# Kernel tuning notes

Measured on AMD Instinct MI355X. Metric: run time of the kernel, lower is better.

## Reference

```python
import jax, jax.numpy as jnp
import numpy as np

DIM = 1024
HEADS = 16
DIM_HEAD = 64
INNER = HEADS * DIM_HEAD
SCALE = 8.0  # default scale in plain_cosine_sim_attention
EPS = 1e-5


def setup_inputs() -> dict:
    key = jax.random.key(0)
    ks = jax.random.split(key, 5)
    b, n = 2, 2048
    x = jax.random.normal(ks[0], (b, n, DIM), dtype=jnp.float32)
    ln_w = jnp.ones((DIM,), dtype=jnp.float32)
    ln_b = jnp.zeros((DIM,), dtype=jnp.float32)
    W_qkv = jax.random.normal(ks[1], (DIM, 3 * INNER), dtype=jnp.float32) * (DIM ** -0.5)
    W_out = jax.random.normal(ks[2], (INNER, DIM), dtype=jnp.float32) * (INNER ** -0.5)
    return {"x": x, "ln_w": ln_w, "ln_b": ln_b, "W_qkv": W_qkv, "W_out": W_out}


def _l2norm(t):
    return t / jnp.clip(jnp.linalg.norm(t, axis=-1, keepdims=True), 1e-12)


def reference(x, ln_w, ln_b, W_qkv, W_out):
    b, n, _ = x.shape
    # LayerNorm
    mu = jnp.mean(x, axis=-1, keepdims=True)
    var = jnp.var(x, axis=-1, keepdims=True)
    xn = (x - mu) * jax.lax.rsqrt(var + EPS) * ln_w + ln_b
    # QKV projection (no bias)
    qkv = xn @ W_qkv  # [b, n, 3*inner]
    q, k, v = jnp.split(qkv, 3, axis=-1)
    # [b, n, h*d] -> [b, h, n, d]
    def to_heads(t):
        return t.reshape(b, n, HEADS, DIM_HEAD).transpose(0, 2, 1, 3)
    q, k, v = to_heads(q), to_heads(k), to_heads(v)
    # cosine-sim attention: l2-normalize q, k then scaled dot product
    q = _l2norm(q)
    k = _l2norm(k)
    sim = jnp.einsum('bhid,bhjd->bhij', q, k) * SCALE
    # causal mask
    causal = jnp.tril(jnp.ones((n, n), dtype=bool))
    sim = jnp.where(causal, sim, jnp.finfo(sim.dtype).min)
    attn = jax.nn.softmax(sim, axis=-1)
    o = jnp.einsum('bhij,bhjd->bhid', attn, v)
    # [b, h, n, d] -> [b, n, h*d]
    o = o.transpose(0, 2, 1, 3).reshape(b, n, INNER)
    return o @ W_out
```

## Files before the change

### kernel.cpp

```cpp
#include <hip/hip_runtime.h>
#include <hip/hip_bf16.h>

typedef __attribute__((ext_vector_type(8))) short short8;
typedef __attribute__((ext_vector_type(4))) float floatx4;

__device__ __forceinline__ ushort f2bf(float f) {
    union { __hip_bfloat16 h; ushort u; } cv;
    cv.h = __float2bfloat16(f);
    return cv.u;
}
__device__ __forceinline__ float bf2f(ushort u) {
    union { ushort u; __hip_bfloat16 h; } cv;
    cv.u = u;
    return __bfloat162float(cv.h);
}
__device__ __forceinline__ ushort f2bf_rtz(float f) {
    union { float f; unsigned u; } cv;
    cv.f = f;
    return (ushort)(cv.u >> 16);
}

typedef __attribute__((address_space(1))) void* gas1_t;
typedef __attribute__((address_space(3))) void* las3_t;
__device__ __forceinline__ void cp16(const ushort* g, ushort* l) {
    __builtin_amdgcn_global_load_lds((gas1_t)(unsigned long long)g,
                                     (las3_t)(unsigned long long)l, 16, 0, 0);
}

__global__ __launch_bounds__(256) void prep_w_ln(const float* __restrict__ Wqkv,
                                                 const float* __restrict__ Wout,
                                                 ushort* __restrict__ WqkvT,
                                                 ushort* __restrict__ WoutT,
                                                 const float* __restrict__ x,
                                                 const float* __restrict__ lw,
                                                 const float* __restrict__ lb,
                                                 ushort* __restrict__ xn) {
    const int id = blockIdx.x;
    const int tid = threadIdx.x;
    if (id < 4096) {
        __shared__ float tile[32][33];
        int bx = id & 127, by = id >> 7;
        const float* in; ushort* out; int R = 1024, C;
        if (bx < 96) { in = Wqkv; out = WqkvT; C = 3072; }
        else { in = Wout; out = WoutT; C = 1024; bx -= 96; }
        int c0 = bx * 32, r0 = by * 32;
        int tx = tid & 31, ty = tid >> 5;
        for (int j = 0; j < 32; j += 8)
            tile[ty + j][tx] = in[(size_t)(r0 + ty + j) * C + c0 + tx];
        __syncthreads();
        for (int j = 0; j < 32; j += 8)
            out[(size_t)(c0 + ty + j) * R + r0 + tx] = f2bf(tile[tx][ty + j]);
    } else {
        int row = id - 4096;
        const float4* xr = (const float4*)(x + (size_t)row * 1024);
        float4 v = xr[tid];
        float s = v.x + v.y + v.z + v.w;
        float sq = v.x * v.x + v.y * v.y + v.z * v.z + v.w * v.w;
        for (int off = 32; off; off >>= 1) {
            s += __shfl_xor(s, off);
            sq += __shfl_xor(sq, off);
        }
        __shared__ float ls[4], lq[4];
        int wave = tid >> 6, lane = tid & 63;
        if (lane == 0) { ls[wave] = s; lq[wave] = sq; }
        __syncthreads();
        s = ls[0] + ls[1] + ls[2] + ls[3];
        sq = lq[0] + lq[1] + lq[2] + lq[3];
        float mu = s * (1.0f / 1024.0f);
        float var = sq * (1.0f / 1024.0f) - mu * mu;
        float rs = rsqrtf(var + 1e-5f);
        const float4* wr = (const float4*)lw;
        const float4* br = (const float4*)lb;
        float4 wv = wr[tid], bv = br[tid];
        ushort4 o;
        o.x = f2bf((v.x - mu) * rs * wv.x + bv.x);
        o.y = f2bf((v.y - mu) * rs * wv.y + bv.y);
        o.z = f2bf((v.z - mu) * rs * wv.z + bv.z);
        o.w = f2bf((v.w - mu) * rs * wv.w + bv.w);
        *(ushort4*)&xn[(size_t)row * 1024 + tid * 4] = o;
    }
}

__global__ __launch_bounds__(256) void gemm_qkv_fused(const ushort* __restrict__ A,
                                                      const ushort* __restrict__ Bt,
                                                      ushort* __restrict__ Qt,
                                                      ushort* __restrict__ Kt,
                                                      ushort* __restrict__ Vb) {
    __shared__ ushort smem[18432];
    const int K = 1024, T = 32;
    const int id = blockIdx.x;
    const int xcd = id & 7, r_ = id >> 3;
    const int bm = (xcd * 4 + r_ / 24) * 128;
    const int bn = r_ % 24;
    const int tid = threadIdx.x;
    const int wave = tid >> 6, lane = tid & 63;
    const int quad = lane >> 4, l15 = lane & 15;
    const int wm = (wave >> 1) * 64, wn = (wave & 1) * 64;

    const int s0 = tid, s1 = tid + 256;
    const int row0 = s0 >> 2, src0 = (s0 & 3) ^ (row0 & 3);
    const int row1 = s1 >> 2, src1 = (s1 & 3) ^ (row1 & 3);

    floatx4 acc[4][4];
    floatx4 z4 = {0.f, 0.f, 0.f, 0.f};
    for (int mi = 0; mi < 4; mi++)
        for (int ni = 0; ni < 4; ni++) acc[mi][ni] = z4;

    const ushort* Ap0 = A + (size_t)(bm + row0) * K + src0 * 8;
    const ushort* Ap1 = A + (size_t)(bm + row1) * K + src1 * 8;
    const ushort* Bp0 = Bt + (size_t)(bn * 128 + row0) * K + src0 * 8;
    const ushort* Bp1 = Bt + (size_t)(bn * 128 + row1) * K + src1 * 8;

    ushort* As = smem;
    ushort* Bs = smem + 8192;

    cp16(Ap0, &As[wave * 512]);
    cp16(Ap1, &As[2048 + wave * 512]);
    cp16(Bp0, &Bs[wave * 512]);
    cp16(Bp1, &Bs[2048 + wave * 512]);

    for (int t = 0; t < T; t++) {
        __syncthreads();
        if (t + 1 < T) {
            const int nb = (t + 1) & 1;
            const int k0n = (t + 1) << 5;
            cp16(Ap0 + k0n, &As[nb * 4096 + wave * 512]);
            cp16(Ap1 + k0n, &As[nb * 4096 + 2048 + wave * 512]);
            cp16(Bp0 + k0n, &Bs[nb * 4096 + wave * 512]);
            cp16(Bp1 + k0n, &Bs[nb * 4096 + 2048 + wave * 512]);
        }
        const ushort* Ab = As + (t & 1) * 4096;
        const ushort* Bb = Bs + (t & 1) * 4096;
        short8 af[4], bfr[4];
        for (int mi = 0; mi < 4; mi++) {
            int ra = wm + mi * 16 + l15;
            af[mi] = *(const short8*)&Ab[ra * 32 + ((quad ^ (ra & 3)) << 3)];
        }
        for (int ni = 0; ni < 4; ni++) {
            int rb = wn + ni * 16 + l15;
            bfr[ni] = *(const short8*)&Bb[rb * 32 + ((quad ^ (rb & 3)) << 3)];
        }
        for (int mi = 0; mi < 4; mi++)
            for (int ni = 0; ni < 4; ni++)
                acc[mi][ni] = __builtin_amdgcn_mfma_f32_16x16x32_bf16(
                    af[mi], bfr[ni], acc[mi][ni], 0, 0, 0);
    }

    const int col_base = bn * 128 + wn;
    const int type = col_base >> 10;
    const int h = (col_base & 1023) >> 6;
    const int row_base = bm + wm;

    if (type < 2) {
        ushort* dst = (type == 0) ? Qt : Kt;
        for (int mi = 0; mi < 4; mi++) {
            for (int r = 0; r < 4; r++) {
                float ss = 0.f;
                for (int ni = 0; ni < 4; ni++) ss += acc[mi][ni][r] * acc[mi][ni][r];
                for (int off = 1; off < 16; off <<= 1) ss += __shfl_xor(ss, off);
                float inv = rsqrtf(fmaxf(ss, 1e-24f));
                int rg = row_base + mi * 16 + quad * 4 + r;
                int bb = rg >> 11, n = rg & 2047;
                size_t orow = ((size_t)(bb * 16 + h) * 2048 + n) * 64;
                for (int ni = 0; ni < 4; ni++)
                    dst[orow + ni * 16 + l15] = f2bf(acc[mi][ni][r] * inv);
            }
        }
    } else {
        __syncthreads();
        ushort* tr = smem + wave * 4608;
        for (int mi = 0; mi < 4; mi++)
            for (int ni = 0; ni < 4; ni++)
                for (int r = 0; r < 4; r++) {
                    int row_l = mi * 16 + quad * 4 + r;
                    int col_l = ni * 16 + l15;
                    tr[col_l * 72 + row_l] = f2bf(acc[mi][ni][r]);
                }
        int bb = row_base >> 11, n0 = row_base & 2047;
        size_t vbase = ((size_t)(bb * 16 + h) * 32 + (n0 >> 6)) * 4096;
        const int dl = lane >> 3, nc = (lane & 7) * 8;
        for (int i = 0; i < 8; i++) {
            int d = dl + i * 8;
            short8 val = *(const short8*)&tr[d * 72 + nc];
            *(short8*)&Vb[vbase + (size_t)d * 64 + nc] = val;
        }
    }
}

__global__ __launch_bounds__(256) void gemm_out(const ushort* __restrict__ A,
                                                const ushort* __restrict__ Bt,
                                                float* __restrict__ C,
                                                int M, int N, int K) {
    __shared__ ushort As[2][128 * 32];
    __shared__ ushort Bs[2][128 * 32];
    const int tid = threadIdx.x;
    const int wave = tid >> 6, lane = tid & 63;
    const int quad = lane >> 4, l15 = lane & 15;
    const int wm = (wave >> 1) * 64, wn = (wave & 1) * 64;
    const int bm = blockIdx.y * 128, bn = blockIdx.x * 128;

    const int s0 = tid, s1 = tid + 256;
    const int row0 = s0 >> 2, src0 = (s0 & 3) ^ (row0 & 3);
    const int row1 = s1 >> 2, src1 = (s1 & 3) ^ (row1 & 3);

    floatx4 acc[4][4];
    floatx4 z4 = {0.f, 0.f, 0.f, 0.f};
    for (int mi = 0; mi < 4; mi++)
        for (int ni = 0; ni < 4; ni++) acc[mi][ni] = z4;

    const ushort* Ap0 = A + (size_t)(bm + row0) * K + src0 * 8;
    const ushort* Ap1 = A + (size_t)(bm + row1) * K + src1 * 8;
    const ushort* Bp0 = Bt + (size_t)(bn + row0) * K + src0 * 8;
    const ushort* Bp1 = Bt + (size_t)(bn + row1) * K + src1 * 8;

    const int T = K >> 5;
    cp16(Ap0, &As[0][wave * 512]);
    cp16(Ap1, &As[0][2048 + wave * 512]);
    cp16(Bp0, &Bs[0][wave * 512]);
    cp16(Bp1, &Bs[0][2048 + wave * 512]);

    for (int t = 0; t < T; t++) {
        __syncthreads();
        if (t + 1 < T) {
            const int nb = (t + 1) & 1;
            const int k0n = (t + 1) << 5;
            cp16(Ap0 + k0n, &As[nb][wave * 512]);
            cp16(Ap1 + k0n, &As[nb][2048 + wave * 512]);
            cp16(Bp0 + k0n, &Bs[nb][wave * 512]);
            cp16(Bp1 + k0n, &Bs[nb][2048 + wave * 512]);
        }
        const ushort* Ab = As[t & 1];
        const ushort* Bb = Bs[t & 1];
        short8 af[4], bfr[4];
        for (int mi = 0; mi < 4; mi++) {
            int ra = wm + mi * 16 + l15;
            af[mi] = *(const short8*)&Ab[ra * 32 + ((quad ^ (ra & 3)) << 3)];
        }
        for (int ni = 0; ni < 4; ni++) {
            int rb = wn + ni * 16 + l15;
            bfr[ni] = *(const short8*)&Bb[rb * 32 + ((quad ^ (rb & 3)) << 3)];
        }
        for (int mi = 0; mi < 4; mi++)
            for (int ni = 0; ni < 4; ni++)
                acc[mi][ni] = __builtin_amdgcn_mfma_f32_16x16x32_bf16(
                    af[mi], bfr[ni], acc[mi][ni], 0, 0, 0);
    }
    for (int mi = 0; mi < 4; mi++)
        for (int ni = 0; ni < 4; ni++)
            for (int r = 0; r < 4; r++) {
                int row = bm + wm + mi * 16 + quad * 4 + r;
                int col = bn + wn + ni * 16 + l15;
                C[(size_t)row * N + col] = acc[mi][ni][r];
            }
}

#define LOG2E8 11.541560327111707f

__global__ __launch_bounds__(256, 1) void flash_attn(const ushort* __restrict__ Qt,
                                                     const ushort* __restrict__ Kt,
                                                     const ushort* __restrict__ Vb,
                                                     ushort* __restrict__ O) {
    const int id = blockIdx.x;
    const int xcd = id & 7, r_ = id >> 3;
    const int bh = xcd * 4 + (r_ >> 3);
    const int pairi = r_ & 7;
    const int b = bh >> 4, h = bh & 15;
    const int tid = threadIdx.x;
    const int wave = tid >> 6, lane = tid & 63;
    const int quad = lane >> 4, l15 = lane & 15;

    __shared__ ushort Ks[2][64 * 64];
    __shared__ ushort Vs[2][64 * 64];
    __shared__ ushort Ps[4][32 * 64];

    const int ch0 = tid, ch1 = tid + 256;
    const int r0 = ch0 >> 3, sg0 = (ch0 & 7) ^ (r0 & 7);
    const int r1 = ch1 >> 3, sg1 = (ch1 & 7) ^ (r1 & 7);

    const ushort* Kp0 = Kt + ((size_t)bh * 2048 + r0) * 64 + sg0 * 8;
    const ushort* Kp1 = Kt + ((size_t)bh * 2048 + r1) * 64 + sg1 * 8;
    const ushort* Vp0 = Vb + (size_t)bh * 131072 + r0 * 64 + sg0 * 8;
    const ushort* Vp1 = Vb + (size_t)bh * 131072 + r1 * 64 + sg1 * 8;

    floatx4 z4 = {0.f, 0.f, 0.f, 0.f};

    for (int pass = 0; pass < 2; pass++) {
        const int st = pass ? (15 - pairi) : pairi;
        const int q0 = st * 128;
        const int ktmax = 2 * st + 1;

        short8 qf[2][2];
        for (int rt = 0; rt < 2; rt++) {
            const ushort* Qp = Qt + ((size_t)bh * 2048 + q0 + wave * 32 + rt * 16 + l15) * 64;
            qf[rt][0] = *(const short8*)(Qp + quad * 8);
            qf[rt][1] = *(const short8*)(Qp + 32 + quad * 8);
        }

        float rs_acc[2][4] = {{0.f, 0.f, 0.f, 0.f}, {0.f, 0.f, 0.f, 0.f}};
        floatx4 o_acc[2][4];
        for (int rt = 0; rt < 2; rt++)
            for (int ni = 0; ni < 4; ni++) o_acc[rt][ni] = z4;

        __syncthreads();
        cp16(Kp0, &Ks[0][wave * 512]);
        cp16(Kp1, &Ks[0][2048 + wave * 512]);
        cp16(Vp0, &Vs[0][wave * 512]);
        cp16(Vp1, &Vs[0][2048 + wave * 512]);

        const int wrow_min = q0 + wave * 32;
        const int wrow_max = wrow_min + 31;

        for (int kt = 0; kt <= ktmax; kt++) {
            const int kv0 = kt * 64;
            __syncthreads();
            if (kt < ktmax) {
                const int nb2 = (kt + 1) & 1;
                const size_t to = (size_t)(kt + 1) * 4096;
                cp16(Kp0 + to, &Ks[nb2][wave * 512]);
                cp16(Kp1 + to, &Ks[nb2][2048 + wave * 512]);
                cp16(Vp0 + to, &Vs[nb2][wave * 512]);
                cp16(Vp1 + to, &Vs[nb2][2048 + wave * 512]);
            }
            if (kv0 > wrow_max) continue;
            const ushort* Kb = Ks[kt & 1];
            const ushort* Vb_ = Vs[kt & 1];

            floatx4 s_acc[2][4];
            for (int rt = 0; rt < 2; rt++)
                for (int ni = 0; ni < 4; ni++) s_acc[rt][ni] = z4;
            for (int ni = 0; ni < 4; ni++) {
                int rb = ni * 16 + l15;
                short8 kf0 = *(const short8*)&Kb[rb * 64 + ((quad ^ (rb & 7)) << 3)];
                short8 kf1 = *(const short8*)&Kb[rb * 64 + (((quad + 4) ^ (rb & 7)) << 3)];
                s_acc[0][ni] = __builtin_amdgcn_mfma_f32_16x16x32_bf16(qf[0][0], kf0, s_acc[0][ni], 0, 0, 0);
                s_acc[0][ni] = __builtin_amdgcn_mfma_f32_16x16x32_bf16(qf[0][1], kf1, s_acc[0][ni], 0, 0, 0);
                s_acc[1][ni] = __builtin_amdgcn_mfma_f32_16x16x32_bf16(qf[1][0], kf0, s_acc[1][ni], 0, 0, 0);
                s_acc[1][ni] = __builtin_amdgcn_mfma_f32_16x16x32_bf16(qf[1][1], kf1, s_acc[1][ni], 0, 0, 0);
            }

            for (int rt = 0; rt < 2; rt++) {
                const int rmin = wrow_min + rt * 16;
                const bool need_mask = (kv0 + 63 > rmin);
                for (int ni = 0; ni < 4; ni++) {
                    const int col_loc = ni * 16 + l15;
                    const int col = kv0 + col_loc;
                    const int chnk = col_loc >> 3;
                    for (int r = 0; r < 4; r++) {
                        const int row_l = rt * 16 + quad * 4 + r;
                        float e = __builtin_amdgcn_exp2f(
                            fmaf(s_acc[rt][ni][r], LOG2E8, -LOG2E8));
                        if (need_mask && col > rmin + quad * 4 + r) e = 0.f;
                        rs_acc[rt][r] += e;
                        Ps[wave][row_l * 64 + (((chnk ^ (row_l & 7)) << 3) | (col_loc & 7))] =
                            f2bf_rtz(e);
                    }
                }
            }

            short8 pa[2][2];
            for (int rt = 0; rt < 2; rt++) {
                int pr = rt * 16 + l15;
                pa[rt][0] = *(const short8*)&Ps[wave][pr * 64 + ((quad ^ (pr & 7)) << 3)];
                pa[rt][1] = *(const short8*)&Ps[wave][pr * 64 + (((quad + 4) ^ (pr & 7)) << 3)];
            }
            for (int ni = 0; ni < 4; ni++) {
                int rv = ni * 16 + l15;
                short8 v0 = *(const short8*)&Vb_[rv * 64 + ((quad ^ (rv & 7)) << 3)];
                short8 v1 = *(const short8*)&Vb_[rv * 64 + (((quad + 4) ^ (rv & 7)) << 3)];
                o_acc[0][ni] = __builtin_amdgcn_mfma_f32_16x16x32_bf16(pa[0][0], v0, o_acc[0][ni], 0, 0, 0);
                o_acc[0][ni] = __builtin_amdgcn_mfma_f32_16x16x32_bf16(pa[0][1], v1, o_acc[0][ni], 0, 0, 0);
                o_acc[1][ni] = __builtin_amdgcn_mfma_f32_16x16x32_bf16(pa[1][0], v0, o_acc[1][ni], 0, 0, 0);
                o_acc[1][ni] = __builtin_amdgcn_mfma_f32_16x16x32_bf16(pa[1][1], v1, o_acc[1][ni], 0, 0, 0);
            }
        }

        for (int rt = 0; rt < 2; rt++) {
            for (int r = 0; r < 4; r++) {
                float rs = rs_acc[rt][r];
                for (int off = 1; off < 16; off <<= 1) rs += __shfl_xor(rs, off);
                float inv = 1.0f / rs;
                int grow = q0 + wave * 32 + rt * 16 + quad * 4 + r;
                size_t rowbase = ((size_t)b * 2048 + grow) * 1024 + h * 64;
                for (int ni = 0; ni < 4; ni++)
                    O[rowbase + ni * 16 + l15] = f2bf(o_acc[rt][ni][r] * inv);
            }
        }
    }
}

extern "C" void kernel_launch(void* const* d_in, const int* in_sizes, int n_in,
                              void* d_out, int out_size, void* d_ws, size_t ws_size,
                              hipStream_t stream) {
    const float* x = (const float*)d_in[0];
    const float* ln_w = (const float*)d_in[1];
    const float* ln_b = (const float*)d_in[2];
    const float* W_qkv = (const float*)d_in[3];
    const float* W_out = (const float*)d_in[4];

    char* w = (char*)d_ws;
    ushort* xn    = (ushort*)(w);
    ushort* WqkvT = (ushort*)(w + (8ull << 20));
    ushort* WoutT = (ushort*)(w + (14ull << 20));
    ushort* Vb    = (ushort*)(w + (16ull << 20));
    ushort* Qt    = (ushort*)(w + (24ull << 20));
    ushort* Kt    = (ushort*)(w + (32ull << 20));
    ushort* obuf  = (ushort*)(w + (40ull << 20));

    prep_w_ln<<<8192, 256, 0, stream>>>(W_qkv, W_out, WqkvT, WoutT, x, ln_w, ln_b, xn);
    gemm_qkv_fused<<<768, 256, 0, stream>>>(xn, WqkvT, Qt, Kt, Vb);
    flash_attn<<<256, 256, 0, stream>>>(Qt, Kt, Vb, obuf);
    gemm_out<<<dim3(8, 32), 256, 0, stream>>>(obuf, WoutT, (float*)d_out, 4096, 1024, 1024);
}
```

Measured before the change: 191.3 us.

## Split attention KV tiles across two blocks and combine partial outputs

```diff
diff --git a/kernel.cpp b/kernel.cpp
--- a/kernel.cpp
+++ b/kernel.cpp
@@ -189,15 +189,18 @@
 
 __global__ __launch_bounds__(256) void gemm_out(const ushort* __restrict__ A,
                                                 const ushort* __restrict__ Bt,
-                                                float* __restrict__ C,
-                                                int M, int N, int K) {
+                                                float* __restrict__ C) {
     __shared__ ushort As[2][128 * 32];
     __shared__ ushort Bs[2][128 * 32];
+    const int K = 1024, N = 1024;
+    const int id = blockIdx.x;
+    const int xcd = id & 7, r_ = id >> 3;
+    const int bm = (xcd * 4 + (r_ >> 3)) * 128;
+    const int bn = (r_ & 7) * 128;
     const int tid = threadIdx.x;
     const int wave = tid >> 6, lane = tid & 63;
     const int quad = lane >> 4, l15 = lane & 15;
     const int wm = (wave >> 1) * 64, wn = (wave & 1) * 64;
-    const int bm = blockIdx.y * 128, bn = blockIdx.x * 128;
 
     const int s0 = tid, s1 = tid + 256;
     const int row0 = s0 >> 2, src0 = (s0 & 3) ^ (row0 & 3);
@@ -256,14 +259,17 @@
 
 #define LOG2E8 11.541560327111707f
 
-__global__ __launch_bounds__(256, 1) void flash_attn(const ushort* __restrict__ Qt,
-                                                     const ushort* __restrict__ Kt,
-                                                     const ushort* __restrict__ Vb,
-                                                     ushort* __restrict__ O) {
+__global__ __launch_bounds__(256) void flash_attn(const ushort* __restrict__ Qt,
+                                                  const ushort* __restrict__ Kt,
+                                                  const ushort* __restrict__ Vb,
+                                                  float* __restrict__ Opart,
+                                                  float* __restrict__ rspart) {
     const int id = blockIdx.x;
     const int xcd = id & 7, r_ = id >> 3;
-    const int bh = xcd * 4 + (r_ >> 3);
-    const int pairi = r_ & 7;
+    const int bh = xcd * 4 + (r_ >> 4);
+    const int rem = r_ & 15;
+    const int pairi = rem >> 1;
+    const int role = rem & 1;
     const int b = bh >> 4, h = bh & 15;
     const int tid = threadIdx.x;
     const int wave = tid >> 6, lane = tid & 63;
@@ -282,12 +288,15 @@
     const ushort* Vp0 = Vb + (size_t)bh * 131072 + r0 * 64 + sg0 * 8;
     const ushort* Vp1 = Vb + (size_t)bh * 131072 + r1 * 64 + sg1 * 8;
 
+    float* Op = Opart + (size_t)role * 4096 * 1024;
+    float* rsp = rspart + (size_t)role * 32 * 2048;
     floatx4 z4 = {0.f, 0.f, 0.f, 0.f};
 
     for (int pass = 0; pass < 2; pass++) {
         const int st = pass ? (15 - pairi) : pairi;
+        const int par = pass ? (1 - role) : role;
         const int q0 = st * 128;
-        const int ktmax = 2 * st + 1;
+        const int nt = st + 1;
 
         short8 qf[2][2];
         for (int rt = 0; rt < 2; rt++) {
@@ -302,28 +311,32 @@
             for (int ni = 0; ni < 4; ni++) o_acc[rt][ni] = z4;
 
         __syncthreads();
-        cp16(Kp0, &Ks[0][wave * 512]);
-        cp16(Kp1, &Ks[0][2048 + wave * 512]);
-        cp16(Vp0, &Vs[0][wave * 512]);
-        cp16(Vp1, &Vs[0][2048 + wave * 512]);
+        {
+            const size_t t0 = (size_t)par * 4096;
+            cp16(Kp0 + t0, &Ks[0][wave * 512]);
+            cp16(Kp1 + t0, &Ks[0][2048 + wave * 512]);
+            cp16(Vp0 + t0, &Vs[0][wave * 512]);
+            cp16(Vp1 + t0, &Vs[0][2048 + wave * 512]);
+        }
 
         const int wrow_min = q0 + wave * 32;
         const int wrow_max = wrow_min + 31;
 
-        for (int kt = 0; kt <= ktmax; kt++) {
+        for (int j = 0; j < nt; j++) {
+            const int kt = par + 2 * j;
             const int kv0 = kt * 64;
             __syncthreads();
-            if (kt < ktmax) {
-                const int nb2 = (kt + 1) & 1;
-                const size_t to = (size_t)(kt + 1) * 4096;
+            if (j + 1 < nt) {
+                const int nb2 = (j + 1) & 1;
+                const size_t to = (size_t)(kt + 2) * 4096;
                 cp16(Kp0 + to, &Ks[nb2][wave * 512]);
                 cp16(Kp1 + to, &Ks[nb2][2048 + wave * 512]);
                 cp16(Vp0 + to, &Vs[nb2][wave * 512]);
                 cp16(Vp1 + to, &Vs[nb2][2048 + wave * 512]);
             }
             if (kv0 > wrow_max) continue;
-            const ushort* Kb = Ks[kt & 1];
-            const ushort* Vb_ = Vs[kt & 1];
+            const ushort* Kb = Ks[j & 1];
+            const ushort* Vb_ = Vs[j & 1];
 
             floatx4 s_acc[2][4];
             for (int rt = 0; rt < 2; rt++)
@@ -378,14 +391,36 @@
             for (int r = 0; r < 4; r++) {
                 float rs = rs_acc[rt][r];
                 for (int off = 1; off < 16; off <<= 1) rs += __shfl_xor(rs, off);
-                float inv = 1.0f / rs;
                 int grow = q0 + wave * 32 + rt * 16 + quad * 4 + r;
+                if (l15 == 0) rsp[(size_t)bh * 2048 + grow] = rs;
                 size_t rowbase = ((size_t)b * 2048 + grow) * 1024 + h * 64;
                 for (int ni = 0; ni < 4; ni++)
-                    O[rowbase + ni * 16 + l15] = f2bf(o_acc[rt][ni][r] * inv);
+                    Op[rowbase + ni * 16 + l15] = o_acc[rt][ni][r];
             }
         }
     }
+}
+
+__global__ __launch_bounds__(256) void combine(const float* __restrict__ Opart,
+                                               const float* __restrict__ rspart,
+                                               ushort* __restrict__ obuf) {
+    const int idx = blockIdx.x * 256 + threadIdx.x;
+    const int row = idx >> 8;
+    const int c4 = (idx & 255) * 4;
+    const size_t off = (size_t)row * 1024 + c4;
+    const int bh = ((row >> 11) << 4) + (c4 >> 6);
+    const int n = row & 2047;
+    const float rs = rspart[(size_t)bh * 2048 + n] +
+                     rspart[(size_t)(32 + bh) * 2048 + n];
+    const float inv = 1.0f / rs;
+    const float4 a = *(const float4*)(Opart + off);
+    const float4 bb = *(const float4*)(Opart + (size_t)4096 * 1024 + off);
+    ushort4 o;
+    o.x = f2bf((a.x + bb.x) * inv);
+    o.y = f2bf((a.y + bb.y) * inv);
+    o.z = f2bf((a.z + bb.z) * inv);
+    o.w = f2bf((a.w + bb.w) * inv);
+    *(ushort4*)&obuf[off] = o;
 }
 
 extern "C" void kernel_launch(void* const* d_in, const int* in_sizes, int n_in,
@@ -398,16 +433,19 @@
     const float* W_out = (const float*)d_in[4];
 
     char* w = (char*)d_ws;
-    ushort* xn    = (ushort*)(w);
-    ushort* WqkvT = (ushort*)(w + (8ull << 20));
-    ushort* WoutT = (ushort*)(w + (14ull << 20));
-    ushort* Vb    = (ushort*)(w + (16ull << 20));
-    ushort* Qt    = (ushort*)(w + (24ull << 20));
-    ushort* Kt    = (ushort*)(w + (32ull << 20));
-    ushort* obuf  = (ushort*)(w + (40ull << 20));
+    ushort* xn     = (ushort*)(w);
+    ushort* WqkvT  = (ushort*)(w + (8ull << 20));
+    ushort* WoutT  = (ushort*)(w + (14ull << 20));
+    ushort* Vb     = (ushort*)(w + (16ull << 20));
+    ushort* Qt     = (ushort*)(w + (24ull << 20));
+    ushort* Kt     = (ushort*)(w + (32ull << 20));
+    ushort* obuf   = (ushort*)(w + (40ull << 20));
+    float*  Opart  = (float*)(w + (48ull << 20));
+    float*  rspart = (float*)(w + (80ull << 20));
 
     prep_w_ln<<<8192, 256, 0, stream>>>(W_qkv, W_out, WqkvT, WoutT, x, ln_w, ln_b, xn);
     gemm_qkv_fused<<<768, 256, 0, stream>>>(xn, WqkvT, Qt, Kt, Vb);
-    flash_attn<<<256, 256, 0, stream>>>(Qt, Kt, Vb, obuf);
-    gemm_out<<<dim3(8, 32), 256, 0, stream>>>(obuf, WoutT, (float*)d_out, 4096, 1024, 1024);
-}
+    flash_attn<<<512, 256, 0, stream>>>(Qt, Kt, Vb, Opart, rspart);
+    combine<<<4096, 256, 0, stream>>>(Opart, rspart, obuf);
+    gemm_out<<<256, 256, 0, stream>>>(obuf, WoutT, (float*)d_out);
+}
```

New measurement: 185.3 us. 3.1% less time.
